# Performance work log

Measured on AMD Instinct MI355X. Metric: run time of the kernel, lower is better.

The kernel has to match this reference:

```python
import jax, jax.numpy as jnp
import numpy as np
from functools import reduce

N_QUBITS = 5
DIM = 2 ** N_QUBITS  # 32


def _cnot_np(c, t):
    # CNOT on N_QUBITS qubits, wire 0 = most significant bit (deepquantum convention)
    M = np.zeros((DIM, DIM), np.complex64)
    for i in range(DIM):
        if (i >> (N_QUBITS - 1 - c)) & 1:
            j = i ^ (1 << (N_QUBITS - 1 - t))
        else:
            j = i
        M[j, i] = 1.0
    return M

_CNOT = {(c, t): jnp.asarray(_cnot_np(c, t))
         for c in range(N_QUBITS) for t in range(N_QUBITS) if c != t}
_EYE2 = jnp.eye(2, dtype=jnp.complex64)


def _ry(theta):
    c = jnp.cos(theta / 2).astype(jnp.complex64)
    s = jnp.sin(theta / 2).astype(jnp.complex64)
    return jnp.stack([jnp.stack([c, -s]), jnp.stack([s, c])])


def _rx(theta):
    c = jnp.cos(theta / 2).astype(jnp.complex64)
    s = jnp.sin(theta / 2).astype(jnp.complex64)
    js = jnp.complex64(1j) * s
    return jnp.stack([jnp.stack([c, -js]), jnp.stack([-js, c])])


def _layer(gate_fn, thetas, wires):
    # kron of single-qubit gates on `wires`, identity elsewhere
    mats, idx = [], 0
    for w in range(N_QUBITS):
        if w in wires:
            mats.append(gate_fn(thetas[idx])); idx += 1
        else:
            mats.append(_EYE2)
    return reduce(jnp.kron, mats)


def _build_circuit(params, wires):
    # params: (n_blocks, 2, len(wires)); block = rylayer, rxlayer, then CNOTs
    # with control = block index and targets = all other wires in increasing order
    U = jnp.eye(DIM, dtype=jnp.complex64)
    n_blocks = params.shape[0]
    for b in range(n_blocks):
        U = _layer(_ry, params[b, 0], wires) @ U
        U = _layer(_rx, params[b, 1], wires) @ U
        for t in wires:
            if t != b:
                U = _CNOT[(b, t)] @ U
    return U


def setup_inputs() -> dict:
    key = jax.random.key(0)
    k1, k2, k3 = jax.random.split(key, 3)
    B = 65536
    oracles = jax.random.normal(k1, (B, DIM, DIM), dtype=jnp.float32)
    params1 = jax.random.normal(k2, (5, 2, 5), dtype=jnp.float32)  # cir1: 5 blocks, ry+rx, 5 wires
    params2 = jax.random.normal(k3, (4, 2, 4), dtype=jnp.float32)  # cir2: 4 blocks, ry+rx, wires [0,1,2,3]
    return {"oracles": oracles, "params1": params1, "params2": params2}


def reference(oracles, params1, params2):
    U1 = _build_circuit(params1, [0, 1, 2, 3, 4])
    U2 = _build_circuit(params2, [0, 1, 2, 3])
    psi1 = U1[:, 0]  # cir1 applied to |00000>
    mid = jnp.einsum('bij,j->bi', oracles.astype(jnp.complex64), psi1)  # oracle application (batched)
    fin = jnp.einsum('ij,bj->bi', U2, mid)                              # cir2
    x = jnp.abs(fin[:, 0]) ** 2 + jnp.abs(fin[:, 1]) ** 2
    return jnp.stack([x, 1.0 - x], axis=-1)  # (B, 2)
```

## Files before the change

kernel.cpp:

```cpp
#include <hip/hip_runtime.h>
#include <math.h>


typedef __fp16 h2 __attribute__((ext_vector_type(2)));
typedef float f4 __attribute__((ext_vector_type(4)));
typedef float f2 __attribute__((ext_vector_type(2)));

#if __has_builtin(__builtin_amdgcn_fdot2)
#define FDOT2(a, b, c) __builtin_amdgcn_fdot2((a), (b), (c), false)
#else
#define FDOT2(a, b, c) ((c) + (float)(a)[0] * (float)(b)[0] + (float)(a)[1] * (float)(b)[1])
#endif

__device__ __forceinline__ h2 pkrtz(float x, float y) {
    return __builtin_amdgcn_cvt_pkrtz(x, y);
}

__device__ __forceinline__ void apply_ry(float c, float s, int mask, int lane,
                                         float& re, float& im) {
    float pre = __shfl_xor(re, mask, 64);
    float pim = __shfl_xor(im, mask, 64);
    float sg = (lane & mask) ? s : -s;
    re = c * re + sg * pre;
    im = c * im + sg * pim;
}

__device__ __forceinline__ void apply_rx(float c, float s, int mask,
                                         float& re, float& im) {
    float pre = __shfl_xor(re, mask, 64);
    float pim = __shfl_xor(im, mask, 64);
    float nre = c * re + s * pim;
    float nim = c * im - s * pre;
    re = nre; im = nim;
}

__device__ __forceinline__ void apply_cnot(int cmask, int tmask, int lane,
                                           float& re, float& im) {
    float pre = __shfl_xor(re, tmask, 64);
    float pim = __shfl_xor(im, tmask, 64);
    if (lane & cmask) { re = pre; im = pim; }
}

struct CF { h2 v[4][4][2]; };

__device__ __forceinline__ void process(const f4& w0, const f4& w1,
                                        const f4& w2, const f4& w3,
                                        const CF& cf, int lane, size_t bb,
                                        float* __restrict__ out) {
    h2 o[4][2];
    o[0][0] = pkrtz(w0.x, w0.y); o[0][1] = pkrtz(w0.z, w0.w);
    o[1][0] = pkrtz(w1.x, w1.y); o[1][1] = pkrtz(w1.z, w1.w);
    o[2][0] = pkrtz(w2.x, w2.y); o[2][1] = pkrtz(w2.z, w2.w);
    o[3][0] = pkrtz(w3.x, w3.y); o[3][1] = pkrtz(w3.z, w3.w);
    float a0 = 0.f, a1 = 0.f, a2 = 0.f, a3 = 0.f;
#pragma unroll
    for (int c = 0; c < 4; ++c) {
        a0 = FDOT2(o[c][0], cf.v[c][0][0], a0); a0 = FDOT2(o[c][1], cf.v[c][0][1], a0);
        a1 = FDOT2(o[c][0], cf.v[c][1][0], a1); a1 = FDOT2(o[c][1], cf.v[c][1][1], a1);
        a2 = FDOT2(o[c][0], cf.v[c][2][0], a2); a2 = FDOT2(o[c][1], cf.v[c][2][1], a2);
        a3 = FDOT2(o[c][0], cf.v[c][3][0], a3); a3 = FDOT2(o[c][1], cf.v[c][3][1], a3);
    }
    float v01 = (lane & 1) ? a1 : a0;
    float q01 = (lane & 1) ? a0 : a1;
    v01 += __shfl_xor(q01, 1, 64);
    float v23 = (lane & 1) ? a3 : a2;
    float q23 = (lane & 1) ? a2 : a3;
    v23 += __shfl_xor(q23, 1, 64);
    float v = (lane & 2) ? v23 : v01;
    float qv = (lane & 2) ? v01 : v23;
    v += __shfl_xor(qv, 2, 64);
#pragma unroll
    for (int m = 4; m < 64; m <<= 1) v += __shfl_xor(v, m, 64);
    float x = v * v;
    x += __shfl_xor(x, 1, 64);
    x += __shfl_xor(x, 2, 64);
    if (lane == 0) {
        f2 res; res.x = x; res.y = 1.0f - x;
        __builtin_nontemporal_store(res, (f2*)out + bb);
    }
}

#define LOADROW(P0, P1, P2, P3, bb) do { if ((size_t)(bb) < end) {           \
    const f4* r_ = (const f4*)(O + (size_t)(bb) * 1024) + lane;              \
    P0 = __builtin_nontemporal_load(r_);                                     \
    P1 = __builtin_nontemporal_load(r_ + 64);                                \
    P2 = __builtin_nontemporal_load(r_ + 128);                               \
    P3 = __builtin_nontemporal_load(r_ + 192); } } while (0)

__global__ __launch_bounds__(256, 4) void fused_kernel(const float* __restrict__ O,
                                                       const float* __restrict__ p1,
                                                       const float* __restrict__ p2,
                                                       float* __restrict__ out,
                                                       int nbatch) {
    const int lane = threadIdx.x & 63;
    const int wid = blockIdx.x * (blockDim.x >> 6) + (threadIdx.x >> 6);
    const int nw = gridDim.x * (blockDim.x >> 6);

    const size_t start = (size_t)wid * (size_t)nbatch / nw;
    const size_t end = (size_t)(wid + 1) * (size_t)nbatch / nw;

    f4 A0, A1, A2, A3, B0, B1, B2, B3, C0, C1, C2, C3;
    LOADROW(A0, A1, A2, A3, start);
    LOADROW(B0, B1, B2, B3, start + 1);
    LOADROW(C0, C1, C2, C3, start + 2);

    float p_re = ((lane & 31) == 0) ? 1.f : 0.f, p_im = 0.f;
    for (int bb = 0; bb < 5; ++bb) {
        for (int w = 0; w < 5; ++w) {
            float s, c; __sincosf(p1[bb * 10 + w] * 0.5f, &s, &c);
            apply_ry(c, s, 1 << (4 - w), lane, p_re, p_im);
        }
        for (int w = 0; w < 5; ++w) {
            float s, c; __sincosf(p1[bb * 10 + 5 + w] * 0.5f, &s, &c);
            apply_rx(c, s, 1 << (4 - w), p_re, p_im);
        }
        for (int t = 0; t < 5; ++t)
            if (t != bb) apply_cnot(1 << (4 - bb), 1 << (4 - t), lane, p_re, p_im);
    }

    float r_re = ((lane & 31) == (lane >> 5)) ? 1.f : 0.f, r_im = 0.f;
    for (int bb = 3; bb >= 0; --bb) {
        for (int t = 3; t >= 0; --t)
            if (t != bb) apply_cnot(1 << (4 - bb), 1 << (4 - t), lane, r_re, r_im);
        for (int w = 0; w < 4; ++w) {
            float s, c; __sincosf(p2[bb * 8 + 4 + w] * 0.5f, &s, &c);
            apply_rx(c, s, 1 << (4 - w), r_re, r_im);
        }
        for (int w = 0; w < 4; ++w) {
            float s, c; __sincosf(p2[bb * 8 + w] * 0.5f, &s, &c);
            apply_ry(c, -s, 1 << (4 - w), lane, r_re, r_im);
        }
    }

    const int tq = (lane >> 3) & 7;
    const int j0 = (4 * lane) & 31;
    float pr[4], pi[4];
#pragma unroll
    for (int k = 0; k < 4; ++k) {
        pr[k] = __shfl(p_re, j0 + k, 64);
        pi[k] = __shfl(p_im, j0 + k, 64);
    }
    CF cf;
#pragma unroll
    for (int c = 0; c < 4; ++c) {
        const int i = 8 * c + tq;
        float ar = __shfl(r_re, i, 64),      ai = __shfl(r_im, i, 64);
        float br = __shfl(r_re, 32 + i, 64), bi = __shfl(r_im, 32 + i, 64);
#pragma unroll
        for (int h = 0; h < 2; ++h) {
            const int k = 2 * h;
            cf.v[c][0][h] = pkrtz(ar * pr[k] - ai * pi[k], ar * pr[k + 1] - ai * pi[k + 1]);
            cf.v[c][1][h] = pkrtz(ar * pi[k] + ai * pr[k], ar * pi[k + 1] + ai * pr[k + 1]);
            cf.v[c][2][h] = pkrtz(br * pr[k] - bi * pi[k], br * pr[k + 1] - bi * pi[k + 1]);
            cf.v[c][3][h] = pkrtz(br * pi[k] + bi * pr[k], br * pi[k + 1] + bi * pr[k + 1]);
        }
    }

    size_t b = start;
    if (b < end) {
        for (;;) {
            process(A0, A1, A2, A3, cf, lane, b, out);
            LOADROW(A0, A1, A2, A3, b + 3);
            if (b + 1 >= end) break;
            process(B0, B1, B2, B3, cf, lane, b + 1, out);
            LOADROW(B0, B1, B2, B3, b + 4);
            if (b + 2 >= end) break;
            process(C0, C1, C2, C3, cf, lane, b + 2, out);
            LOADROW(C0, C1, C2, C3, b + 5);
            b += 3;
            if (b >= end) break;
        }
    }
}

extern "C" void kernel_launch(void* const* d_in, const int* in_sizes, int n_in,
                              void* d_out, int out_size, void* d_ws, size_t ws_size,
                              hipStream_t stream) {
    const float* oracles = (const float*)d_in[0];
    const float* p1 = (const float*)d_in[1];
    const float* p2 = (const float*)d_in[2];
    float* out = (float*)d_out;
    int nbatch = in_sizes[0] / 1024;

    fused_kernel<<<1024, 256, 0, stream>>>(oracles, p1, p2, out, nbatch);
}
```

Baseline: 55.01 us.

## Interleave batch rows across waves, deepen prefetch to four rows, drop nontemporal hints

Each wave now takes batch rows strided by the total wave count instead of a contiguous chunk, so concurrent waves read neighbouring 4 KB rows. The software prefetch ring grows from three to four in-flight rows per wave. Nontemporal load and store builtins are replaced with ordinary accesses. These changes aim to improve DRAM access locality and hide more memory latency in this bandwidth-bound kernel, at the cost of extra registers per wave and possible cache pollution from the streamed oracle data.

```diff
diff --git a/kernel.cpp b/kernel.cpp
--- a/kernel.cpp
+++ b/kernel.cpp
@@ -76,16 +76,13 @@
     x += __shfl_xor(x, 2, 64);
     if (lane == 0) {
         f2 res; res.x = x; res.y = 1.0f - x;
-        __builtin_nontemporal_store(res, (f2*)out + bb);
+        ((f2*)out)[bb] = res;
     }
 }
 
-#define LOADROW(P0, P1, P2, P3, bb) do { if ((size_t)(bb) < end) {           \
-    const f4* r_ = (const f4*)(O + (size_t)(bb) * 1024) + lane;              \
-    P0 = __builtin_nontemporal_load(r_);                                     \
-    P1 = __builtin_nontemporal_load(r_ + 64);                                \
-    P2 = __builtin_nontemporal_load(r_ + 128);                               \
-    P3 = __builtin_nontemporal_load(r_ + 192); } } while (0)
+#define LOADROW(P0, P1, P2, P3, it) do { if ((it) < cnt) {                     \
+    const f4* r_ = (const f4*)(O + ((size_t)wid + (size_t)(it) * nw) * 1024) + lane; \
+    P0 = r_[0]; P1 = r_[64]; P2 = r_[128]; P3 = r_[192]; } } while (0)
 
 __global__ __launch_bounds__(256, 4) void fused_kernel(const float* __restrict__ O,
                                                        const float* __restrict__ p1,
@@ -95,14 +92,13 @@
     const int lane = threadIdx.x & 63;
     const int wid = blockIdx.x * (blockDim.x >> 6) + (threadIdx.x >> 6);
     const int nw = gridDim.x * (blockDim.x >> 6);
+    const int cnt = (nbatch > wid) ? (nbatch - wid + nw - 1) / nw : 0;
 
-    const size_t start = (size_t)wid * (size_t)nbatch / nw;
-    const size_t end = (size_t)(wid + 1) * (size_t)nbatch / nw;
-
-    f4 A0, A1, A2, A3, B0, B1, B2, B3, C0, C1, C2, C3;
-    LOADROW(A0, A1, A2, A3, start);
-    LOADROW(B0, B1, B2, B3, start + 1);
-    LOADROW(C0, C1, C2, C3, start + 2);
+    f4 A0, A1, A2, A3, B0, B1, B2, B3, C0, C1, C2, C3, D0, D1, D2, D3;
+    LOADROW(A0, A1, A2, A3, 0);
+    LOADROW(B0, B1, B2, B3, 1);
+    LOADROW(C0, C1, C2, C3, 2);
+    LOADROW(D0, D1, D2, D3, 3);
 
     float p_re = ((lane & 31) == 0) ? 1.f : 0.f, p_im = 0.f;
     for (int bb = 0; bb < 5; ++bb) {
@@ -156,20 +152,23 @@
         }
     }
 
-    size_t b = start;
-    if (b < end) {
-        for (;;) {
-            process(A0, A1, A2, A3, cf, lane, b, out);
-            LOADROW(A0, A1, A2, A3, b + 3);
-            if (b + 1 >= end) break;
-            process(B0, B1, B2, B3, cf, lane, b + 1, out);
-            LOADROW(B0, B1, B2, B3, b + 4);
-            if (b + 2 >= end) break;
-            process(C0, C1, C2, C3, cf, lane, b + 2, out);
-            LOADROW(C0, C1, C2, C3, b + 5);
-            b += 3;
-            if (b >= end) break;
-        }
+    if (cnt == 0) return;
+
+    int it = 0;
+    for (;;) {
+        process(A0, A1, A2, A3, cf, lane, (size_t)wid + (size_t)it * nw, out);
+        LOADROW(A0, A1, A2, A3, it + 4);
+        if (it + 1 >= cnt) break;
+        process(B0, B1, B2, B3, cf, lane, (size_t)wid + (size_t)(it + 1) * nw, out);
+        LOADROW(B0, B1, B2, B3, it + 5);
+        if (it + 2 >= cnt) break;
+        process(C0, C1, C2, C3, cf, lane, (size_t)wid + (size_t)(it + 2) * nw, out);
+        LOADROW(C0, C1, C2, C3, it + 6);
+        if (it + 3 >= cnt) break;
+        process(D0, D1, D2, D3, cf, lane, (size_t)wid + (size_t)(it + 3) * nw, out);
+        LOADROW(D0, D1, D2, D3, it + 7);
+        it += 4;
+        if (it >= cnt) break;
     }
 }
 
```

Result: faster. 47.80 us (-13.1%).
